# Performance work log

Hardware: AMD Instinct MI355X
Metric: run time of the kernel (lower is better)

## Reference

```python
import jax, jax.numpy as jnp
import numpy as np

N_CHEM = 200000
N_GENE = 20000
N_EDGES = 1000000
IN, HID, OUT = 128, 256, 128


def _seg_mean(msg, dst, num_segments):
    # DGL fn.mean: mean of incoming messages; nodes with zero in-degree get 0.
    s = jax.ops.segment_sum(msg, dst, num_segments=num_segments)
    cnt = jax.ops.segment_sum(jnp.ones((msg.shape[0],), msg.dtype), dst,
                              num_segments=num_segments)[:, None]
    return jnp.where(cnt > 0, s / jnp.maximum(cnt, 1.0), 0.0)


def setup_inputs() -> dict:
    key = jax.random.key(0)
    ks = jax.random.split(key, 12)
    d = {
        'src_cg': jax.random.randint(ks[0], (N_EDGES,), 0, N_CHEM, dtype=jnp.int32),
        'dst_cg': jax.random.randint(ks[1], (N_EDGES,), 0, N_GENE, dtype=jnp.int32),
        'src_gc': jax.random.randint(ks[2], (N_EDGES,), 0, N_GENE, dtype=jnp.int32),
        'dst_gc': jax.random.randint(ks[3], (N_EDGES,), 0, N_CHEM, dtype=jnp.int32),
        'embed_chem': jax.random.normal(ks[4], (N_CHEM, IN), jnp.float32) * 0.1,
        'embed_gene': jax.random.normal(ks[5], (N_GENE, IN), jnp.float32) * 0.1,
        'W1_cg': jax.random.normal(ks[6], (IN, HID), jnp.float32) * (1.0 / np.sqrt(IN)),
        'b1_cg': jnp.zeros((HID,), jnp.float32),
        'W1_gc': jax.random.normal(ks[7], (IN, HID), jnp.float32) * (1.0 / np.sqrt(IN)),
        'b1_gc': jnp.zeros((HID,), jnp.float32),
        'W2_cg': jax.random.normal(ks[8], (HID, OUT), jnp.float32) * (1.0 / np.sqrt(HID)),
        'b2_cg': jnp.zeros((OUT,), jnp.float32),
        'W2_gc': jax.random.normal(ks[9], (HID, OUT), jnp.float32) * (1.0 / np.sqrt(HID)),
        'b2_gc': jnp.zeros((OUT,), jnp.float32),
    }
    return d


def _layer(h_chem, h_gene, W_cg, b_cg, W_gc, b_gc, src_cg, dst_cg, src_gc, dst_gc):
    # per-etype linear transform on source features
    Wh_cg = h_chem @ W_cg + b_cg   # [N_CHEM, D]
    Wh_gc = h_gene @ W_gc + b_gc   # [N_GENE, D]
    # copy_u + mean per etype; multi_update_all('sum') -> single etype per dst here
    new_gene = _seg_mean(Wh_cg[src_cg], dst_cg, N_GENE)
    new_chem = _seg_mean(Wh_gc[src_gc], dst_gc, N_CHEM)
    return new_chem, new_gene


def reference(src_cg, dst_cg, src_gc, dst_gc, embed_chem, embed_gene,
              W1_cg, b1_cg, W1_gc, b1_gc, W2_cg, b2_cg, W2_gc, b2_gc):
    h_chem, h_gene = _layer(embed_chem, embed_gene, W1_cg, b1_cg, W1_gc, b1_gc,
                            src_cg, dst_cg, src_gc, dst_gc)
    h_chem = jax.nn.leaky_relu(h_chem, negative_slope=0.01)
    h_gene = jax.nn.leaky_relu(h_gene, negative_slope=0.01)
    h_chem, _ = _layer(h_chem, h_gene, W2_cg, b2_cg, W2_gc, b2_gc,
                       src_cg, dst_cg, src_gc, dst_gc)
    return h_chem  # [N_CHEM, OUT]
```

## Files before the change

kernel.cpp:

```cpp
#include <hip/hip_runtime.h>
#include <stdint.h>
#include <stddef.h>

#define N_CHEM 200000
#define N_GENE 20000
#define N_EDGES 1000000
#define IN_D 128
#define HID_D 256
#define OUT_D 128
#define N_SEG (N_GENE + N_CHEM)

#define NGB 313
#define NCB 391
#define NB  (NGB + NCB)
#define EPB 4096
#define CAP 8192
#define DROPPED 0x80000000

typedef float nfloat4 __attribute__((ext_vector_type(4)));
typedef __attribute__((ext_vector_type(8))) short bf16x8;
typedef __attribute__((ext_vector_type(4))) float f32x4;

__device__ inline unsigned bf16rne(float x) {
    unsigned u = __float_as_uint(x);
    return (u + 0x7FFFu + ((u >> 16) & 1u)) >> 16;
}

__device__ inline int bucket_of(int slot) {
    return (slot < N_GENE) ? (slot >> 6) : (NGB + ((slot - N_GENE) >> 9));
}
__device__ inline int bucket_slot0(int b) {
    return (b < NGB) ? (b << 6) : (N_GENE + ((b - NGB) << 9));
}


__global__ __launch_bounds__(256) void place_convert_kernel(
        const int* __restrict__ src_cg, const int* __restrict__ dst_cg,
        const int* __restrict__ src_gc, const int* __restrict__ dst_gc,
        int* __restrict__ bcur, unsigned* __restrict__ records,
        const float* __restrict__ conv_in, unsigned short* __restrict__ conv_out,
        int nba) {
    if ((int)blockIdx.x >= nba) {
        int cb = blockIdx.x - nba;
        const int tid = threadIdx.x;
        #pragma unroll
        for (int q = 0; q < 4; ++q) {
            int i = cb * 1024 + q * 256 + tid;
            if (i < N_CHEM * IN_D / 4) {
                float4 v = *(const float4*)&conv_in[(size_t)i * 4];
                uint2 w;
                w.x = bf16rne(v.x) | (bf16rne(v.y) << 16);
                w.y = bf16rne(v.z) | (bf16rne(v.w) << 16);
                *(uint2*)&conv_out[(size_t)i * 4] = w;
            }
        }
        return;
    }
    __shared__ unsigned stage_rec[EPB];
    __shared__ unsigned short stage_bkt[EPB];
    __shared__ int hist[NB];
    __shared__ int excl[NB];
    __shared__ int cursor[NB];
    __shared__ int Dofs[NB];
    __shared__ int tsum[256];
    const int tid = threadIdx.x;
    const int e0 = blockIdx.x * EPB;
    const int cnt_blk = min(EPB, 2 * N_EDGES - e0);

    for (int i = tid; i < NB; i += 256) hist[i] = 0;
    __syncthreads();

    int slotR[EPB / 256], srcR[EPB / 256];
    #pragma unroll
    for (int q = 0; q < EPB / 256; ++q) {
        int e = e0 + q * 256 + tid;
        int slot = -1, s = 0;
        if (e < N_EDGES)            { slot = dst_cg[e];                    s = src_cg[e]; }
        else if (e < 2 * N_EDGES)   { slot = N_GENE + dst_gc[e - N_EDGES]; s = src_gc[e - N_EDGES]; }
        slotR[q] = slot; srcR[q] = s;
        if (slot >= 0) atomicAdd(&hist[bucket_of(slot)], 1);
    }
    __syncthreads();

    const int b3 = tid * 3;
    int h0 = (b3     < NB) ? hist[b3]     : 0;
    int h1 = (b3 + 1 < NB) ? hist[b3 + 1] : 0;
    int h2 = (b3 + 2 < NB) ? hist[b3 + 2] : 0;
    int ts = h0 + h1 + h2;
    tsum[tid] = ts;
    __syncthreads();
    for (int off = 1; off < 256; off <<= 1) {
        int t = (tid >= off) ? tsum[tid - off] : 0;
        __syncthreads();
        tsum[tid] += t;
        __syncthreads();
    }
    int base = tsum[tid] - ts;
    if (b3     < NB) { excl[b3]     = base;           cursor[b3]     = base; }
    if (b3 + 1 < NB) { excl[b3 + 1] = base + h0;      cursor[b3 + 1] = base + h0; }
    if (b3 + 2 < NB) { excl[b3 + 2] = base + h0 + h1; cursor[b3 + 2] = base + h0 + h1; }
    __syncthreads();

    #pragma unroll
    for (int q = 0; q < EPB / 256; ++q) {
        int slot = slotR[q];
        if (slot >= 0) {
            int b = bucket_of(slot);
            int p = atomicAdd(&cursor[b], 1);
            stage_rec[p] = ((unsigned)(slot - bucket_slot0(b)) << 18) | (unsigned)srcR[q];
            stage_bkt[p] = (unsigned short)b;
        }
    }
    __syncthreads();

    for (int i = tid; i < NB; i += 256) {
        int n = hist[i];
        if (n) {
            int got = atomicAdd(&bcur[i], n);
            Dofs[i] = (got + n <= CAP) ? (i * CAP + got - excl[i]) : (int)DROPPED;
        }
    }
    __syncthreads();

    for (int i = tid; i < cnt_blk; i += 256) {
        int d = Dofs[stage_bkt[i]];
        if (d != (int)DROPPED) records[i + d] = stage_rec[i];
    }
}


__global__ void bucket_scan_kernel(const int* __restrict__ bcur,
                                   int* __restrict__ bbase, int* __restrict__ indptr) {
    __shared__ int sm[1024];
    const int tid = threadIdx.x;
    int v = (tid < NB) ? min(bcur[tid], CAP) : 0;
    sm[tid] = v;
    __syncthreads();
    for (int off = 1; off < 1024; off <<= 1) {
        int t = (tid >= off) ? sm[tid - off] : 0;
        __syncthreads();
        sm[tid] += t;
        __syncthreads();
    }
    if (tid < NB) bbase[tid] = sm[tid] - v;
    if (tid == NB - 1) {
        bbase[NB] = sm[tid];
        indptr[N_SEG] = sm[tid];
    }
}


__global__ __launch_bounds__(256) void bin_b_kernel(
        const unsigned* __restrict__ records, const int* __restrict__ bbase,
        const int* __restrict__ bcur,
        int* __restrict__ indptr, int* __restrict__ esrc) {
    __shared__ int hist[512];
    __shared__ int tsum[256];
    const int tid = threadIdx.x;
    const int b = blockIdx.x;
    int slot0 = bucket_slot0(b);
    int nslots = (b < NGB) ? min(64, N_GENE - slot0) : min(512, N_SEG - slot0);
    const int rbase = bbase[b];
    const int E = min(bcur[b], CAP);
    const unsigned* rec = &records[(size_t)b * CAP];

    hist[tid] = 0; hist[tid + 256] = 0;
    __syncthreads();
    for (int i = tid; i < E; i += 256)
        atomicAdd(&hist[rec[i] >> 18], 1);
    __syncthreads();

    int h0 = hist[2 * tid], h1 = hist[2 * tid + 1];
    int ts = h0 + h1;
    tsum[tid] = ts;
    __syncthreads();
    for (int off = 1; off < 256; off <<= 1) {
        int t = (tid >= off) ? tsum[tid - off] : 0;
        __syncthreads();
        tsum[tid] += t;
        __syncthreads();
    }
    int ex = tsum[tid] - ts;
    __syncthreads();
    hist[2 * tid]     = ex;
    hist[2 * tid + 1] = ex + h0;
    if (2 * tid     < nslots) indptr[slot0 + 2 * tid]     = rbase + ex;
    if (2 * tid + 1 < nslots) indptr[slot0 + 2 * tid + 1] = rbase + ex + h0;
    __syncthreads();

    for (int i = tid; i < E; i += 256) {
        unsigned r = rec[i];
        int p = atomicAdd(&hist[r >> 18], 1);
        esrc[rbase + p] = (int)(r & 0x3FFFFu);
    }
}


__device__ inline void acc_u(float* a, uint4 v) {
    a[0] += __uint_as_float(v.x << 16); a[1] += __uint_as_float(v.x & 0xffff0000u);
    a[2] += __uint_as_float(v.y << 16); a[3] += __uint_as_float(v.y & 0xffff0000u);
    a[4] += __uint_as_float(v.z << 16); a[5] += __uint_as_float(v.z & 0xffff0000u);
    a[6] += __uint_as_float(v.w << 16); a[7] += __uint_as_float(v.w & 0xffff0000u);
}


__global__ __launch_bounds__(256) void gather_mean_bf16_split_kernel(
        const unsigned short* __restrict__ table,
        const int* __restrict__ indptr, const int* __restrict__ esrc,
        unsigned short* __restrict__ outb, int n) {
    int lane = threadIdx.x & 15;
    int half = (threadIdx.x >> 4) & 1;
    int node = blockIdx.x * 8 + (threadIdx.x >> 5);
    if (node >= n) return;
    int s = indptr[node], e = indptr[node + 1];
    int deg = e - s;
    int mid = s + ((deg + 1) >> 1);
    int j0 = half ? mid : s;
    int j1 = half ? e   : mid;
    int c = lane << 3;
    float acc[8] = {};
    int j = j0;
    for (; j + 8 <= j1; j += 8) {
        int i0 = esrc[j],     i1 = esrc[j + 1], i2 = esrc[j + 2], i3 = esrc[j + 3];
        int i4 = esrc[j + 4], i5 = esrc[j + 5], i6 = esrc[j + 6], i7 = esrc[j + 7];
        uint4 v0 = *(const uint4*)&table[(size_t)i0 * 128 + c];
        uint4 v1 = *(const uint4*)&table[(size_t)i1 * 128 + c];
        uint4 v2 = *(const uint4*)&table[(size_t)i2 * 128 + c];
        uint4 v3 = *(const uint4*)&table[(size_t)i3 * 128 + c];
        uint4 v4 = *(const uint4*)&table[(size_t)i4 * 128 + c];
        uint4 v5 = *(const uint4*)&table[(size_t)i5 * 128 + c];
        uint4 v6 = *(const uint4*)&table[(size_t)i6 * 128 + c];
        uint4 v7 = *(const uint4*)&table[(size_t)i7 * 128 + c];
        acc_u(acc, v0); acc_u(acc, v1); acc_u(acc, v2); acc_u(acc, v3);
        acc_u(acc, v4); acc_u(acc, v5); acc_u(acc, v6); acc_u(acc, v7);
    }
    for (; j + 4 <= j1; j += 4) {
        uint4 v0 = *(const uint4*)&table[(size_t)esrc[j]     * 128 + c];
        uint4 v1 = *(const uint4*)&table[(size_t)esrc[j + 1] * 128 + c];
        uint4 v2 = *(const uint4*)&table[(size_t)esrc[j + 2] * 128 + c];
        uint4 v3 = *(const uint4*)&table[(size_t)esrc[j + 3] * 128 + c];
        acc_u(acc, v0); acc_u(acc, v1); acc_u(acc, v2); acc_u(acc, v3);
    }
    for (; j < j1; ++j) {
        uint4 v = *(const uint4*)&table[(size_t)esrc[j] * 128 + c];
        acc_u(acc, v);
    }
    #pragma unroll
    for (int q = 0; q < 8; ++q) acc[q] += __shfl_xor(acc[q], 16);
    if (half == 0) {
        float inv = (deg > 0) ? 1.f / (float)deg : 0.f;
        #pragma unroll
        for (int q = 0; q < 8; ++q) acc[q] *= inv;
        uint4 w;
        w.x = bf16rne(acc[0]) | (bf16rne(acc[1]) << 16);
        w.y = bf16rne(acc[2]) | (bf16rne(acc[3]) << 16);
        w.z = bf16rne(acc[4]) | (bf16rne(acc[5]) << 16);
        w.w = bf16rne(acc[6]) | (bf16rne(acc[7]) << 16);
        *(uint4*)&outb[(size_t)node * 128 + c] = w;
    }
}


template<bool NT>
__global__ __launch_bounds__(256) void gather_mean_bf16_kernel(
        const unsigned short* __restrict__ table,
        const int* __restrict__ indptr, const int* __restrict__ esrc,
        float* __restrict__ out, int n) {
    int lane = threadIdx.x & 15;
    int node = blockIdx.x * 16 + (threadIdx.x >> 4);
    if (node >= n) return;
    int s = indptr[node], e = indptr[node + 1];
    int c = lane << 3;
    float acc[8] = {};
    int j = s;
    for (; j + 4 <= e; j += 4) {
        uint4 v0 = *(const uint4*)&table[(size_t)esrc[j]     * 128 + c];
        uint4 v1 = *(const uint4*)&table[(size_t)esrc[j + 1] * 128 + c];
        uint4 v2 = *(const uint4*)&table[(size_t)esrc[j + 2] * 128 + c];
        uint4 v3 = *(const uint4*)&table[(size_t)esrc[j + 3] * 128 + c];
        acc_u(acc, v0); acc_u(acc, v1); acc_u(acc, v2); acc_u(acc, v3);
    }
    for (; j < e; ++j) {
        uint4 v = *(const uint4*)&table[(size_t)esrc[j] * 128 + c];
        acc_u(acc, v);
    }
    int deg = e - s;
    float inv = (deg > 0) ? 1.f / (float)deg : 0.f;
    #pragma unroll
    for (int q = 0; q < 8; ++q) acc[q] *= inv;
    float* dst = &out[(size_t)node * 128 + c];
    if (NT) {
        nfloat4 a = { acc[0], acc[1], acc[2], acc[3] };
        nfloat4 b = { acc[4], acc[5], acc[6], acc[7] };
        __builtin_nontemporal_store(a, (nfloat4*)dst);
        __builtin_nontemporal_store(b, (nfloat4*)(dst + 4));
    } else {
        *(float4*)dst       = make_float4(acc[0], acc[1], acc[2], acc[3]);
        *(float4*)(dst + 4) = make_float4(acc[4], acc[5], acc[6], acc[7]);
    }
}


__global__ __launch_bounds__(256) void gather_mean_f32_kernel(
        const float* __restrict__ table,
        const int* __restrict__ indptr, const int* __restrict__ esrc,
        float* __restrict__ out, int n) {
    int lane = threadIdx.x & 31;
    int node = blockIdx.x * 8 + (threadIdx.x >> 5);
    if (node >= n) return;
    int s = indptr[node], e = indptr[node + 1];
    int c = lane << 2;
    float4 acc = make_float4(0.f, 0.f, 0.f, 0.f);
    int j = s;
    for (; j + 4 <= e; j += 4) {
        int s0 = esrc[j], s1 = esrc[j + 1], s2 = esrc[j + 2], s3 = esrc[j + 3];
        float4 v0 = *(const float4*)&table[(size_t)s0 * 128 + c];
        float4 v1 = *(const float4*)&table[(size_t)s1 * 128 + c];
        float4 v2 = *(const float4*)&table[(size_t)s2 * 128 + c];
        float4 v3 = *(const float4*)&table[(size_t)s3 * 128 + c];
        acc.x += (v0.x + v1.x) + (v2.x + v3.x);
        acc.y += (v0.y + v1.y) + (v2.y + v3.y);
        acc.z += (v0.z + v1.z) + (v2.z + v3.z);
        acc.w += (v0.w + v1.w) + (v2.w + v3.w);
    }
    for (; j < e; ++j) {
        float4 v = *(const float4*)&table[(size_t)esrc[j] * 128 + c];
        acc.x += v.x; acc.y += v.y; acc.z += v.z; acc.w += v.w;
    }
    int deg = e - s;
    float inv = (deg > 0) ? 1.f / (float)deg : 0.f;
    acc.x *= inv; acc.y *= inv; acc.z *= inv; acc.w *= inv;
    *(float4*)&out[(size_t)node * 128 + c] = acc;
}


template<int K, int N, bool MASK_LEAKY>
__global__ __launch_bounds__(256) void gemm_mfma_kernel(
        const unsigned short* __restrict__ A,
        const float* __restrict__ W,
        const float* __restrict__ bias,
        const int* __restrict__ indptr,
        unsigned short* __restrict__ C,
        int M) {
    constexpr int BK  = 128;
    constexpr int LDK = BK + 8;
    __shared__ unsigned short As[64 * LDK];
    __shared__ unsigned short Ws[64 * LDK];
    const int tid  = threadIdx.x;
    const int lane = tid & 63;
    const int w    = tid >> 6;
    const int m0 = blockIdx.x * 64;
    const int n0 = blockIdx.y * 64;
    const int l15 = lane & 15;
    const int lhi = lane >> 4;
    f32x4 acc[4] = {};

    for (int kt0 = 0; kt0 < K; kt0 += BK) {
        #pragma unroll
        for (int it = 0; it < 4; ++it) {
            int idx = it * 256 + tid;
            int row = idx >> 4;
            int c8  = (idx & 15) << 3;
            uint4 v = make_uint4(0u, 0u, 0u, 0u);
            if (m0 + row < M)
                v = *(const uint4*)&A[(size_t)(m0 + row) * K + kt0 + c8];
            *(uint4*)&As[row * LDK + c8] = v;
        }
        #pragma unroll
        for (int it = 0; it < 32; ++it) {
            int i = it * 256 + tid;
            int k = i >> 6;
            int n = i & 63;
            float f = W[(size_t)(kt0 + k) * N + n0 + n];
            Ws[n * LDK + k] = (unsigned short)bf16rne(f);
        }
        __syncthreads();

        #pragma unroll
        for (int kk = 0; kk < BK; kk += 32) {
            bf16x8 a = *(const bf16x8*)&As[(w * 16 + l15) * LDK + kk + lhi * 8];
            #pragma unroll
            for (int nt = 0; nt < 4; ++nt) {
                bf16x8 b = *(const bf16x8*)&Ws[(nt * 16 + l15) * LDK + kk + lhi * 8];
                acc[nt] = __builtin_amdgcn_mfma_f32_16x16x32_bf16(a, b, acc[nt], 0, 0, 0);
            }
        }
        __syncthreads();
    }

    #pragma unroll
    for (int nt = 0; nt < 4; ++nt) {
        int col = n0 + nt * 16 + l15;
        float bz = bias[col];
        #pragma unroll
        for (int r = 0; r < 4; ++r) {
            int row = m0 + w * 16 + lhi * 4 + r;
            if (row < M) {
                float v = acc[nt][r] + bz;
                if (MASK_LEAKY) {
                    int deg = indptr[row + 1] - indptr[row];
                    v = (deg == 0) ? 0.f : (v > 0.f ? v : 0.01f * v);
                }
                C[(size_t)row * N + col] = (unsigned short)bf16rne(v);
            }
        }
    }
}


template<int K, int N, bool MASK_LEAKY, bool BF16_OUT>
__global__ __launch_bounds__(256) void gemm_kernel(const float* __restrict__ A,
                                                   const float* __restrict__ W,
                                                   const float* __restrict__ bias,
                                                   const int* __restrict__ indptr,
                                                   void* __restrict__ Cout, int M) {
    __shared__ float As[64 * 68];
    __shared__ float Ws[64 * 64];
    const int tid = threadIdx.x;
    const int tx = tid & 15, ty = tid >> 4;
    const int m0 = blockIdx.x * 64;
    const int n0 = blockIdx.y * 64;
    const int r0 = ty << 2, c0 = tx << 2;
    float acc[4][4] = {};

    for (int kt = 0; kt < K; kt += 64) {
        #pragma unroll
        for (int q = 0; q < 4; ++q) {
            int idx = tid + q * 256;
            int row = idx >> 4;
            int c4  = (idx & 15) << 2;
            float4 v = make_float4(0.f, 0.f, 0.f, 0.f);
            if (m0 + row < M)
                v = *(const float4*)&A[(size_t)(m0 + row) * K + kt + c4];
            *(float4*)&As[row * 68 + c4] = v;
        }
        #pragma unroll
        for (int q = 0; q < 4; ++q) {
            int idx = tid + q * 256;
            int k   = idx >> 4;
            int c4  = (idx & 15) << 2;
            *(float4*)&Ws[(k << 6) + c4] =
                *(const float4*)&W[(size_t)(kt + k) * N + n0 + c4];
        }
        __syncthreads();

        #pragma unroll 4
        for (int k = 0; k < 64; k += 4) {
            float a[4][4];
            #pragma unroll
            for (int r = 0; r < 4; ++r) {
                float4 v = *(const float4*)&As[(r0 + r) * 68 + k];
                a[r][0] = v.x; a[r][1] = v.y; a[r][2] = v.z; a[r][3] = v.w;
            }
            #pragma unroll
            for (int kk = 0; kk < 4; ++kk) {
                float4 w = *(const float4*)&Ws[((k + kk) << 6) + c0];
                #pragma unroll
                for (int r = 0; r < 4; ++r) {
                    acc[r][0] = fmaf(a[r][kk], w.x, acc[r][0]);
                    acc[r][1] = fmaf(a[r][kk], w.y, acc[r][1]);
                    acc[r][2] = fmaf(a[r][kk], w.z, acc[r][2]);
                    acc[r][3] = fmaf(a[r][kk], w.w, acc[r][3]);
                }
            }
        }
        __syncthreads();
    }

    float4 b = *(const float4*)&bias[n0 + c0];
    #pragma unroll
    for (int r = 0; r < 4; ++r) {
        int row = m0 + r0 + r;
        if (row < M) {
            float4 v;
            v.x = acc[r][0] + b.x; v.y = acc[r][1] + b.y;
            v.z = acc[r][2] + b.z; v.w = acc[r][3] + b.w;
            if (MASK_LEAKY) {
                int deg = indptr[row + 1] - indptr[row];
                if (deg == 0) {
                    v = make_float4(0.f, 0.f, 0.f, 0.f);
                } else {
                    v.x = v.x > 0.f ? v.x : 0.01f * v.x;
                    v.y = v.y > 0.f ? v.y : 0.01f * v.y;
                    v.z = v.z > 0.f ? v.z : 0.01f * v.z;
                    v.w = v.w > 0.f ? v.w : 0.01f * v.w;
                }
            }
            if (BF16_OUT) {
                uint2 w;
                w.x = bf16rne(v.x) | (bf16rne(v.y) << 16);
                w.y = bf16rne(v.z) | (bf16rne(v.w) << 16);
                *(uint2*)&((unsigned short*)Cout)[(size_t)row * N + n0 + c0] = w;
            } else {
                *(float4*)&((float*)Cout)[(size_t)row * N + n0 + c0] = v;
            }
        }
    }
}


extern "C" void kernel_launch(void* const* d_in, const int* in_sizes, int n_in,
                              void* d_out, int out_size, void* d_ws, size_t ws_size,
                              hipStream_t stream) {
    const int*   src_cg     = (const int*)d_in[0];
    const int*   dst_cg     = (const int*)d_in[1];
    const int*   src_gc     = (const int*)d_in[2];
    const int*   dst_gc     = (const int*)d_in[3];
    const float* embed_chem = (const float*)d_in[4];
    const float* W1_cg = (const float*)d_in[6];
    const float* b1_cg = (const float*)d_in[7];
    const float* W2_gc = (const float*)d_in[12];
    const float* b2_gc = (const float*)d_in[13];
    float* out = (float*)d_out;

    int* ws_i = (int*)d_ws;
    size_t off = 0;
    int* bcur  = ws_i + off; off += NB;
    int* bbase = ws_i + off; off += NB + 1;
    off = (off + 3) & ~(size_t)3;
    int* indptr = ws_i + off; off += N_SEG + 1; off = (off + 3) & ~(size_t)3;
    int* esrc   = ws_i + off; off += 2 * N_EDGES;
    size_t union_off = off;
    unsigned* records = (unsigned*)(ws_i + union_off);
    unsigned short* agg1b   = (unsigned short*)(ws_i + union_off);
    unsigned short* h_geneb = agg1b + (size_t)N_GENE * IN_D;
    float* agg1f   = (float*)(ws_i + union_off);
    float* h_genef = agg1f + (size_t)N_GENE * IN_D;
    size_t union_sz = (size_t)N_GENE * (IN_D + HID_D);
    off = union_off + union_sz;
    unsigned short* Wh2b = (unsigned short*)(ws_i + off); off += (size_t)N_GENE * OUT_D / 2;
    unsigned short* embedb = (unsigned short*)(ws_i + off);
    size_t off_full = off + (size_t)N_CHEM * IN_D / 2;
    const bool bf16_embed = ws_size >= off_full * sizeof(int);

    (void)hipMemsetAsync(bcur, 0, NB * sizeof(int), stream);

    const int nba = (2 * N_EDGES + EPB - 1) / EPB;
    const int nconv = bf16_embed ? (N_CHEM * IN_D / 4 + 1023) / 1024 : 0;
    place_convert_kernel<<<nba + nconv, 256, 0, stream>>>(
        src_cg, dst_cg, src_gc, dst_gc, bcur, records, embed_chem, embedb, nba);
    bucket_scan_kernel<<<1, 1024, 0, stream>>>(bcur, bbase, indptr);
    bin_b_kernel<<<NB, 256, 0, stream>>>(records, bbase, bcur, indptr, esrc);

    if (bf16_embed) {
        gather_mean_bf16_split_kernel<<<(N_GENE + 7) / 8, 256, 0, stream>>>(
            embedb, indptr, esrc, agg1b, N_GENE);
        {
            dim3 g((N_GENE + 63) / 64, HID_D / 64), blk(256);
            gemm_mfma_kernel<IN_D, HID_D, true><<<g, blk, 0, stream>>>(
                agg1b, W1_cg, b1_cg, indptr, h_geneb, N_GENE);
        }
        {
            dim3 g((N_GENE + 63) / 64, OUT_D / 64), blk(256);
            gemm_mfma_kernel<HID_D, OUT_D, false><<<g, blk, 0, stream>>>(
                h_geneb, W2_gc, b2_gc, nullptr, Wh2b, N_GENE);
        }
    } else {
        gather_mean_f32_kernel<<<(N_GENE + 7) / 8, 256, 0, stream>>>(
            embed_chem, indptr, esrc, agg1f, N_GENE);
        {
            dim3 g((N_GENE + 63) / 64, HID_D / 64), blk(256);
            gemm_kernel<IN_D, HID_D, true, false><<<g, blk, 0, stream>>>(
                agg1f, W1_cg, b1_cg, indptr, h_genef, N_GENE);
        }
        {
            dim3 g((N_GENE + 63) / 64, OUT_D / 64), blk(256);
            gemm_kernel<HID_D, OUT_D, false, true><<<g, blk, 0, stream>>>(
                h_genef, W2_gc, b2_gc, nullptr, Wh2b, N_GENE);
        }
    }

    gather_mean_bf16_kernel<true><<<(N_CHEM + 15) / 16, 256, 0, stream>>>(
        Wh2b, indptr + N_GENE, esrc, out, N_CHEM);
}
```

Measured before the change: 379.3 us.

## Fuse bucket scan into place kernel via last-block pattern, move bf16 convert

The separate single-block bucket scan kernel is removed; the last place block to finish, detected through an atomic done counter after a threadfence, computes the bucket prefix sums instead. The embed bf16 conversion moves from the place kernel into the bin_b kernel launch, and edges per block drop from 4096 to 2048 to raise block count and cut shared memory. This saves one launch and rebalances work, in exchange for a serial tail on the last block and smaller per-block batches that issue more global atomics on bucket counters.

```diff
diff --git a/kernel.cpp b/kernel.cpp
--- a/kernel.cpp
+++ b/kernel.cpp
@@ -13,7 +13,8 @@
 #define NGB 313
 #define NCB 391
 #define NB  (NGB + NCB)
-#define EPB 4096
+#define EPB 2048
+#define NBA ((2 * N_EDGES + EPB - 1) / EPB)
 #define CAP 8192
 #define DROPPED 0x80000000
 
@@ -34,35 +35,17 @@
 }
 
 
-__global__ __launch_bounds__(256) void place_convert_kernel(
+__global__ __launch_bounds__(256) void place_kernel(
         const int* __restrict__ src_cg, const int* __restrict__ dst_cg,
         const int* __restrict__ src_gc, const int* __restrict__ dst_gc,
         int* __restrict__ bcur, unsigned* __restrict__ records,
-        const float* __restrict__ conv_in, unsigned short* __restrict__ conv_out,
-        int nba) {
-    if ((int)blockIdx.x >= nba) {
-        int cb = blockIdx.x - nba;
-        const int tid = threadIdx.x;
-        #pragma unroll
-        for (int q = 0; q < 4; ++q) {
-            int i = cb * 1024 + q * 256 + tid;
-            if (i < N_CHEM * IN_D / 4) {
-                float4 v = *(const float4*)&conv_in[(size_t)i * 4];
-                uint2 w;
-                w.x = bf16rne(v.x) | (bf16rne(v.y) << 16);
-                w.y = bf16rne(v.z) | (bf16rne(v.w) << 16);
-                *(uint2*)&conv_out[(size_t)i * 4] = w;
-            }
-        }
-        return;
-    }
+        int* __restrict__ done, int* __restrict__ bbase, int* __restrict__ indptr) {
     __shared__ unsigned stage_rec[EPB];
     __shared__ unsigned short stage_bkt[EPB];
     __shared__ int hist[NB];
-    __shared__ int excl[NB];
     __shared__ int cursor[NB];
-    __shared__ int Dofs[NB];
     __shared__ int tsum[256];
+    __shared__ int is_last;
     const int tid = threadIdx.x;
     const int e0 = blockIdx.x * EPB;
     const int cnt_blk = min(EPB, 2 * N_EDGES - e0);
@@ -96,9 +79,9 @@
         __syncthreads();
     }
     int base = tsum[tid] - ts;
-    if (b3     < NB) { excl[b3]     = base;           cursor[b3]     = base; }
-    if (b3 + 1 < NB) { excl[b3 + 1] = base + h0;      cursor[b3 + 1] = base + h0; }
-    if (b3 + 2 < NB) { excl[b3 + 2] = base + h0 + h1; cursor[b3 + 2] = base + h0 + h1; }
+    if (b3     < NB) cursor[b3]     = base;
+    if (b3 + 1 < NB) cursor[b3 + 1] = base + h0;
+    if (b3 + 2 < NB) cursor[b3 + 2] = base + h0 + h1;
     __syncthreads();
 
     #pragma unroll
@@ -117,43 +100,67 @@
         int n = hist[i];
         if (n) {
             int got = atomicAdd(&bcur[i], n);
-            Dofs[i] = (got + n <= CAP) ? (i * CAP + got - excl[i]) : (int)DROPPED;
+            int excl_i = cursor[i] - n;
+            hist[i] = (got + n <= CAP) ? (i * CAP + got - excl_i) : (int)DROPPED;
         }
     }
     __syncthreads();
 
     for (int i = tid; i < cnt_blk; i += 256) {
-        int d = Dofs[stage_bkt[i]];
+        int d = hist[stage_bkt[i]];
         if (d != (int)DROPPED) records[i + d] = stage_rec[i];
     }
-}
-
-
-__global__ void bucket_scan_kernel(const int* __restrict__ bcur,
-                                   int* __restrict__ bbase, int* __restrict__ indptr) {
-    __shared__ int sm[1024];
-    const int tid = threadIdx.x;
-    int v = (tid < NB) ? min(bcur[tid], CAP) : 0;
-    sm[tid] = v;
-    __syncthreads();
-    for (int off = 1; off < 1024; off <<= 1) {
-        int t = (tid >= off) ? sm[tid - off] : 0;
-        __syncthreads();
-        sm[tid] += t;
-        __syncthreads();
-    }
-    if (tid < NB) bbase[tid] = sm[tid] - v;
-    if (tid == NB - 1) {
-        bbase[NB] = sm[tid];
-        indptr[N_SEG] = sm[tid];
-    }
-}
-
-
-__global__ __launch_bounds__(256) void bin_b_kernel(
+
+    __threadfence();
+    __syncthreads();
+    if (tid == 0) is_last = (atomicAdd(done, 1) == NBA - 1);
+    __syncthreads();
+    if (!is_last) return;
+
+    int v0 = (b3     < NB) ? min(atomicAdd(&bcur[b3],     0), CAP) : 0;
+    int v1 = (b3 + 1 < NB) ? min(atomicAdd(&bcur[b3 + 1], 0), CAP) : 0;
+    int v2 = (b3 + 2 < NB) ? min(atomicAdd(&bcur[b3 + 2], 0), CAP) : 0;
+    ts = v0 + v1 + v2;
+    tsum[tid] = ts;
+    __syncthreads();
+    for (int off = 1; off < 256; off <<= 1) {
+        int t = (tid >= off) ? tsum[tid - off] : 0;
+        __syncthreads();
+        tsum[tid] += t;
+        __syncthreads();
+    }
+    base = tsum[tid] - ts;
+    if (b3     < NB) bbase[b3]     = base;
+    if (b3 + 1 < NB) bbase[b3 + 1] = base + v0;
+    if (b3 + 2 < NB) bbase[b3 + 2] = base + v0 + v1;
+    if (tid == 255) {
+        bbase[NB] = tsum[255];
+        indptr[N_SEG] = tsum[255];
+    }
+}
+
+
+__global__ __launch_bounds__(256) void bin_b_convert_kernel(
         const unsigned* __restrict__ records, const int* __restrict__ bbase,
         const int* __restrict__ bcur,
-        int* __restrict__ indptr, int* __restrict__ esrc) {
+        int* __restrict__ indptr, int* __restrict__ esrc,
+        const float* __restrict__ conv_in, unsigned short* __restrict__ conv_out) {
+    if ((int)blockIdx.x >= NB) {
+        int cb = blockIdx.x - NB;
+        const int tid = threadIdx.x;
+        #pragma unroll
+        for (int q = 0; q < 4; ++q) {
+            int i = cb * 1024 + q * 256 + tid;
+            if (i < N_CHEM * IN_D / 4) {
+                float4 v = *(const float4*)&conv_in[(size_t)i * 4];
+                uint2 w;
+                w.x = bf16rne(v.x) | (bf16rne(v.y) << 16);
+                w.y = bf16rne(v.z) | (bf16rne(v.w) << 16);
+                *(uint2*)&conv_out[(size_t)i * 4] = w;
+            }
+        }
+        return;
+    }
     __shared__ int hist[512];
     __shared__ int tsum[256];
     const int tid = threadIdx.x;
@@ -516,6 +523,7 @@
     int* ws_i = (int*)d_ws;
     size_t off = 0;
     int* bcur  = ws_i + off; off += NB;
+    int* done  = ws_i + off; off += 1;
     int* bbase = ws_i + off; off += NB + 1;
     off = (off + 3) & ~(size_t)3;
     int* indptr = ws_i + off; off += N_SEG + 1; off = (off + 3) & ~(size_t)3;
@@ -533,14 +541,13 @@
     size_t off_full = off + (size_t)N_CHEM * IN_D / 2;
     const bool bf16_embed = ws_size >= off_full * sizeof(int);
 
-    (void)hipMemsetAsync(bcur, 0, NB * sizeof(int), stream);
-
-    const int nba = (2 * N_EDGES + EPB - 1) / EPB;
+    (void)hipMemsetAsync(bcur, 0, (NB + 1) * sizeof(int), stream);
+
+    place_kernel<<<NBA, 256, 0, stream>>>(src_cg, dst_cg, src_gc, dst_gc,
+                                          bcur, records, done, bbase, indptr);
     const int nconv = bf16_embed ? (N_CHEM * IN_D / 4 + 1023) / 1024 : 0;
-    place_convert_kernel<<<nba + nconv, 256, 0, stream>>>(
-        src_cg, dst_cg, src_gc, dst_gc, bcur, records, embed_chem, embedb, nba);
-    bucket_scan_kernel<<<1, 1024, 0, stream>>>(bcur, bbase, indptr);
-    bin_b_kernel<<<NB, 256, 0, stream>>>(records, bbase, bcur, indptr, esrc);
+    bin_b_convert_kernel<<<NB + nconv, 256, 0, stream>>>(
+        records, bbase, bcur, indptr, esrc, embed_chem, embedb);
 
     if (bf16_embed) {
         gather_mean_bf16_split_kernel<<<(N_GENE + 7) / 8, 256, 0, stream>>>(
```

After: 518.0 us. 36.5% more time.
